# Kernel tuning notes

Hardware: AMD Instinct MI355X
Metric: run time of the kernel (lower is better)

## Reference

```python
import jax, jax.numpy as jnp
import numpy as np

B, S, E = 4, 2048, 1024
H = 16
DH = E // H  # per-head qk and v projection dim (64)


def setup_inputs() -> dict:
    key = jax.random.key(0)
    ks = jax.random.split(key, 12)
    sc = lambda fan_in: 1.0 / np.sqrt(fan_in)
    inp = {
        "query": jax.random.normal(ks[0], (B, S, E), jnp.float32),
        "key": jax.random.normal(ks[1], (B, S, E), jnp.float32),
        "value": jax.random.normal(ks[2], (B, S, E), jnp.float32),
        "attention_bias": jax.random.normal(ks[3], (S, S), jnp.float32),
        # stacked per-head Linear weights/biases (H independent heads in original)
        "Wq": jax.random.uniform(ks[4], (H, E, DH), jnp.float32, -sc(E), sc(E)),
        "bq": jax.random.uniform(ks[5], (H, DH), jnp.float32, -sc(E), sc(E)),
        "Wk": jax.random.uniform(ks[6], (H, E, DH), jnp.float32, -sc(E), sc(E)),
        "bk": jax.random.uniform(ks[7], (H, DH), jnp.float32, -sc(E), sc(E)),
        "Wv": jax.random.uniform(ks[8], (H, E, DH), jnp.float32, -sc(E), sc(E)),
        "bv": jax.random.uniform(ks[9], (H, DH), jnp.float32, -sc(E), sc(E)),
        "Wo": jax.random.uniform(ks[10], (H * DH, E), jnp.float32, -sc(H * DH), sc(H * DH)),
        "bo": jax.random.uniform(ks[11], (E,), jnp.float32, -sc(H * DH), sc(H * DH)),
    }
    return inp


def reference(query, key, value, attention_bias, Wq, bq, Wk, bk, Wv, bv, Wo, bo):
    # Batched equivalent of per-head Linear projections + per-head SDPA.
    q = jnp.einsum("bse,hed->bhsd", query, Wq) + bq[None, :, None, :]   # (B,H,S,DH)
    k = jnp.einsum("bte,hed->bhtd", key, Wk) + bk[None, :, None, :]     # (B,H,S,DH)
    v = jnp.einsum("bte,hed->bhtd", value, Wv) + bv[None, :, None, :]   # (B,H,S,DH)
    scale = 1.0 / jnp.sqrt(jnp.asarray(DH, q.dtype))
    scores = jnp.einsum("bhsd,bhtd->bhst", q, k) * scale                # (B,H,S,S)
    scores = scores + attention_bias[None, None, :, :]
    attn = jax.nn.softmax(scores, axis=-1)
    # dropout_p = 0.0 -> no dropout
    ctx = jnp.einsum("bhst,bhtd->bhsd", attn, v)                        # (B,H,S,DH)
    concat = ctx.transpose(0, 2, 1, 3).reshape(B, S, H * DH)            # (B,S,H*DH)
    return concat @ Wo + bo                                             # (B,S,E)
```

## Files before the change

### kernel.cpp

```cpp
#include <hip/hip_runtime.h>

#define S_LEN 2048
#define E_DIM 1024
#define H_NUM 16

typedef __attribute__((ext_vector_type(8))) short s16x8;
typedef __attribute__((ext_vector_type(4))) float f32x4;
typedef __attribute__((ext_vector_type(4))) _Float16 h16x4;
typedef __attribute__((ext_vector_type(8))) _Float16 h16x8;

#define GA(p) ((__attribute__((address_space(1))) void*)(p))
#define LA(p) ((__attribute__((address_space(3))) void*)(p))

#define LOG2E 1.4426950408889634f
#define SCALE_Q (0.125f * LOG2E)
#define SHIFT 12.0f

union cvt16 { int4 v; s16x8 s8; short e[8]; };

__device__ __forceinline__ short f2bf(float f) {
  union { float f; unsigned u; } v; v.f = f;
  unsigned r = v.u + 0x7FFFu + ((v.u >> 16) & 1u);
  return (short)(r >> 16);
}
__device__ __forceinline__ short f2bf_fast(float f) {
  union { float f; unsigned u; } v; v.f = f;
  return (short)((v.u + 0x8000u) >> 16);
}
__device__ __forceinline__ unsigned pk2(float lo, float hi) {
  return (unsigned)(unsigned short)f2bf_fast(lo) |
         ((unsigned)(unsigned short)f2bf_fast(hi) << 16);
}

__global__ void transpose_cast(const float* __restrict__ src, short* __restrict__ dst,
                               int R, int C, long sbs, long dbs, float scale) {
  __shared__ float tile[32][33];
  const float* s = src + (long)blockIdx.z * sbs;
  short* d = dst + (long)blockIdx.z * dbs;
  int c0 = blockIdx.x * 32, r0 = blockIdx.y * 32;
  #pragma unroll
  for (int i = threadIdx.y; i < 32; i += 8)
    tile[i][threadIdx.x] = s[(long)(r0 + i) * C + c0 + threadIdx.x];
  __syncthreads();
  #pragma unroll
  for (int i = threadIdx.y; i < 32; i += 8)
    d[(long)(c0 + i) * R + r0 + threadIdx.x] = f2bf(tile[threadIdx.x][i] * scale);
}

__global__ void bias_rearrange(const float* __restrict__ bias, _Float16* __restrict__ biasR) {
  long g = (long)blockIdx.x * 256 + threadIdx.x;
  int q    = (int)(g >> 8);
  int kv   = ((int)(g >> 3)) & 31;
  int quad = ((int)(g >> 1)) & 3;
  int c    = (int)g & 1;
  const float* src = bias + (long)q * 2048 + kv * 64 + c * 32 + quad * 4;
  f32x4 lo = *(const f32x4*)(src);
  f32x4 hi = *(const f32x4*)(src + 16);
  h16x8 hv;
  #pragma unroll
  for (int e = 0; e < 4; ++e) { hv[e] = (_Float16)lo[e]; hv[4 + e] = (_Float16)hi[e]; }
  *(h16x8*)(biasR + g * 8) = hv;
}

__global__ __launch_bounds__(256, 3) void proj_gemm(
    const float* __restrict__ Aq, const float* __restrict__ Ak, const float* __restrict__ Av,
    const short* __restrict__ Bt,
    const float* __restrict__ bq, const float* __restrict__ bk, const float* __restrict__ bv,
    short* __restrict__ qkOut, short* __restrict__ VT) {
  __shared__ float Asub[128 * 64];
  __shared__ short Bsub[128 * 64];
  const int tid = threadIdx.x;
  const int w = tid >> 6, lane = tid & 63, ln = lane & 15, quad = lane >> 4;
  const int row0 = blockIdx.x * 128, n0 = blockIdx.y * 128;
  const int seg = n0 >> 10;
  const float* A = (seg == 0) ? Aq : ((seg == 1) ? Ak : Av);
  const float* bptr = (seg == 0) ? bq : ((seg == 1) ? bk : bv);
  const float bscale = (seg == 0) ? SCALE_Q : 1.0f;
  const int nloc = n0 & 1023;
  const int wm = (w & 1) * 64, wn = (w >> 1) * 64;

  f32x4 acc[4][4];
  #pragma unroll
  for (int i = 0; i < 4; ++i)
    #pragma unroll
    for (int j = 0; j < 4; ++j) acc[i][j] = (f32x4){0.f, 0.f, 0.f, 0.f};

  for (int kt = 0; kt < 16; ++kt) {
    const int k0 = kt * 64;
    #pragma unroll
    for (int j = 0; j < 4; ++j) {
      int ci = (w * 4 + j) * 64 + lane;
      int r = ci >> 3, s = ci & 7, g = s ^ (r & 7);
      const short* gb = Bt + (long)(n0 + r) * 1024 + k0 + g * 8;
      __builtin_amdgcn_global_load_lds(GA(gb), LA(&Bsub[ci * 8]), 16, 0, 0);
    }
    #pragma unroll
    for (int it = 0; it < 8; ++it) {
      int ci = it * 256 + tid;
      int r = ci >> 4, s = ci & 15, g = (s & 8) | ((s & 7) ^ (r & 7));
      const float* ga = A + (long)(row0 + r) * 1024 + k0 + g * 4;
      __builtin_amdgcn_global_load_lds(GA(ga), LA(&Asub[ci * 4]), 16, 0, 0);
    }
    __syncthreads();
    #pragma unroll
    for (int kk = 0; kk < 2; ++kk) {
      s16x8 af[4], bfr[4];
      #pragma unroll
      for (int i = 0; i < 4; ++i) {
        int ra = wm + i * 16 + ln;
        int c0 = kk * 8 + quad * 2;
        int s0 = (c0 & 8) | ((c0 & 7) ^ (ra & 7));
        int c1 = c0 + 1;
        int s1 = (c1 & 8) | ((c1 & 7) ^ (ra & 7));
        f32x4 lo = *(const f32x4*)&Asub[ra * 64 + s0 * 4];
        f32x4 hi = *(const f32x4*)&Asub[ra * 64 + s1 * 4];
        s16x8 t;
        t[0] = f2bf(lo[0]); t[1] = f2bf(lo[1]); t[2] = f2bf(lo[2]); t[3] = f2bf(lo[3]);
        t[4] = f2bf(hi[0]); t[5] = f2bf(hi[1]); t[6] = f2bf(hi[2]); t[7] = f2bf(hi[3]);
        af[i] = t;
      }
      #pragma unroll
      for (int j = 0; j < 4; ++j) {
        int rb = wn + j * 16 + ln;
        int slot = (kk * 4 + quad) ^ (rb & 7);
        bfr[j] = *(const s16x8*)&Bsub[rb * 64 + slot * 8];
      }
      #pragma unroll
      for (int i = 0; i < 4; ++i)
        #pragma unroll
        for (int j = 0; j < 4; ++j)
          acc[i][j] = __builtin_amdgcn_mfma_f32_16x16x32_bf16(af[i], bfr[j], acc[i][j], 0, 0, 0);
    }
    __syncthreads();
  }
  if (seg < 2) {
    #pragma unroll
    for (int j = 0; j < 4; ++j) {
      float bvj = bptr[nloc + wn + j * 16 + ln] * bscale;
      int n = n0 + wn + j * 16 + ln;
      #pragma unroll
      for (int i = 0; i < 4; ++i)
        #pragma unroll
        for (int r = 0; r < 4; ++r) {
          int row = row0 + wm + i * 16 + quad * 4 + r;
          qkOut[(long)row * 2048 + n] = f2bf(acc[i][j][r] + bvj);
        }
    }
  } else {
    #pragma unroll
    for (int j = 0; j < 4; ++j) {
      int nl = nloc + wn + j * 16 + ln;
      int hh = nl >> 6, d = nl & 63;
      float bvj = bptr[nl];
      #pragma unroll
      for (int i = 0; i < 4; ++i) {
        int row = row0 + wm + i * 16 + quad * 4;
        int b = row >> 11, t = row & 2047;
        int u = t & 63;
        int pt = (t & ~63) | (u & 0x23) | ((u & 0x10) >> 2) | ((u & 0x0C) << 1);
        short4 sv;
        sv.x = f2bf(acc[i][j][0] + bvj);
        sv.y = f2bf(acc[i][j][1] + bvj);
        sv.z = f2bf(acc[i][j][2] + bvj);
        sv.w = f2bf(acc[i][j][3] + bvj);
        *(short4*)&VT[((long)(b * 16 + hh) * 64 + d) * 2048 + pt] = sv;
      }
    }
  }
}

__global__ __launch_bounds__(256, 3) void flash_attn(
    const short* __restrict__ qk, const short* __restrict__ VT,
    const _Float16* __restrict__ biasR, short* __restrict__ concat) {
  __shared__ short Ks[2][4096];
  __shared__ short Vs[2][4096];
  const int tid = threadIdx.x;
  const int w = tid >> 6, lane = tid & 63, ln = lane & 15, quad = lane >> 4;
  const int q0 = blockIdx.x * 128;
  const int h = blockIdx.y, bb = blockIdx.z;

  s16x8 ones;
  #pragma unroll
  for (int e = 0; e < 8; ++e) ones[e] = (short)0x3F80;

  s16x8 qf[2][2];
  const short* qbase = qk + (long)(bb * 2048 + q0 + w * 32) * 2048 + h * 64;
  #pragma unroll
  for (int i = 0; i < 2; ++i)
    #pragma unroll
    for (int kk = 0; kk < 2; ++kk) {
      cvt16 u; u.v = *(const int4*)(qbase + (long)(i * 16 + ln) * 2048 + kk * 32 + quad * 8);
      qf[i][kk] = u.s8;
    }

  f32x4 o[2][4], lacc[2];
  #pragma unroll
  for (int i = 0; i < 2; ++i) {
    #pragma unroll
    for (int nt = 0; nt < 4; ++nt) o[i][nt] = (f32x4){0.f, 0.f, 0.f, 0.f};
    lacc[i] = (f32x4){0.f, 0.f, 0.f, 0.f};
  }

  const short* kbase = qk + (long)bb * 2048 * 2048 + 1024 + h * 64;
  const short* vbase = VT + (long)(bb * 16 + h) * 64 * 2048;
  const _Float16* bbase = biasR + (long)(q0 + w * 32 + ln) * 2048 + quad * 16;

  #pragma unroll
  for (int j = 0; j < 2; ++j) {
    int ci = (w * 2 + j) * 64 + lane;
    int r = ci >> 3, cs = (ci & 7) ^ (r & 7);
    __builtin_amdgcn_global_load_lds(GA(kbase + (long)r * 2048 + cs * 8), LA(&Ks[0][(w * 2 + j) * 512]), 16, 0, 0);
    __builtin_amdgcn_global_load_lds(GA(vbase + (long)r * 2048 + cs * 8), LA(&Vs[0][(w * 2 + j) * 512]), 16, 0, 0);
  }

  for (int kv = 0; kv < 32; ++kv) {
    const int t0 = kv * 64, b = kv & 1;
    __syncthreads();

    h16x8 bld[2][2];
    #pragma unroll
    for (int i = 0; i < 2; ++i)
      #pragma unroll
      for (int c = 0; c < 2; ++c)
        bld[i][c] = *(const h16x8*)(bbase + (long)i * 16 * 2048 + kv * 64 + c * 8);
    __builtin_amdgcn_sched_barrier(0);

    if (kv < 31) {
      const short* kb = kbase + (long)(t0 + 64) * 2048;
      const short* vb = vbase + (t0 + 64);
      #pragma unroll
      for (int j = 0; j < 2; ++j) {
        int ci = (w * 2 + j) * 64 + lane;
        int r = ci >> 3, cs = (ci & 7) ^ (r & 7);
        __builtin_amdgcn_global_load_lds(GA(kb + (long)r * 2048 + cs * 8), LA(&Ks[b ^ 1][(w * 2 + j) * 512]), 16, 0, 0);
        __builtin_amdgcn_global_load_lds(GA(vb + (long)r * 2048 + cs * 8), LA(&Vs[b ^ 1][(w * 2 + j) * 512]), 16, 0, 0);
      }
    }

    f32x4 sa[2][4];
    #pragma unroll
    for (int i = 0; i < 2; ++i)
      #pragma unroll
      for (int nt = 0; nt < 4; ++nt) sa[i][nt] = (f32x4){-SHIFT, -SHIFT, -SHIFT, -SHIFT};
    #pragma unroll
    for (int kk = 0; kk < 2; ++kk) {
      s16x8 bfr[4];
      #pragma unroll
      for (int nt = 0; nt < 4; ++nt)
        bfr[nt] = *(const s16x8*)&Ks[b][((nt * 16 + ln) << 6) + (((kk * 4 + quad) ^ (ln & 7)) << 3)];
      __builtin_amdgcn_s_setprio(1);
      #pragma unroll
      for (int i = 0; i < 2; ++i)
        #pragma unroll
        for (int nt = 0; nt < 4; ++nt)
          sa[i][nt] = __builtin_amdgcn_mfma_f32_16x16x32_bf16(bfr[nt], qf[i][kk], sa[i][nt], 0, 0, 0);
      __builtin_amdgcn_s_setprio(0);
    }

    s16x8 pa[2][2];
    #pragma unroll
    for (int i = 0; i < 2; ++i) {
      #pragma unroll
      for (int nt = 0; nt < 4; ++nt) {
        #pragma unroll
        for (int r = 0; r < 4; ++r) {
          float bv = (float)bld[i][nt >> 1][(nt & 1) * 4 + r];
          sa[i][nt][r] = __builtin_amdgcn_exp2f(fmaf(bv, LOG2E, sa[i][nt][r]));
        }
      }
      #pragma unroll
      for (int kk = 0; kk < 2; ++kk) {
        union { unsigned u[4]; s16x8 v; } pw;
        pw.u[0] = pk2(sa[i][2 * kk][0], sa[i][2 * kk][1]);
        pw.u[1] = pk2(sa[i][2 * kk][2], sa[i][2 * kk][3]);
        pw.u[2] = pk2(sa[i][2 * kk + 1][0], sa[i][2 * kk + 1][1]);
        pw.u[3] = pk2(sa[i][2 * kk + 1][2], sa[i][2 * kk + 1][3]);
        pa[i][kk] = pw.v;
      }
    }

    #pragma unroll
    for (int kk = 0; kk < 2; ++kk) {
      s16x8 vbf[4];
      #pragma unroll
      for (int nt = 0; nt < 4; ++nt)
        vbf[nt] = *(const s16x8*)&Vs[b][((nt * 16 + ln) << 6) + (((kk * 4 + quad) ^ (ln & 7)) << 3)];
      __builtin_amdgcn_s_setprio(1);
      #pragma unroll
      for (int i = 0; i < 2; ++i) {
        #pragma unroll
        for (int nt = 0; nt < 4; ++nt)
          o[i][nt] = __builtin_amdgcn_mfma_f32_16x16x32_bf16(pa[i][kk], vbf[nt], o[i][nt], 0, 0, 0);
        lacc[i] = __builtin_amdgcn_mfma_f32_16x16x32_bf16(pa[i][kk], ones, lacc[i], 0, 0, 0);
      }
      __builtin_amdgcn_s_setprio(0);
    }
  }

  #pragma unroll
  for (int i = 0; i < 2; ++i) {
    float inv[4];
    #pragma unroll
    for (int r = 0; r < 4; ++r) inv[r] = __builtin_amdgcn_rcpf(lacc[i][r]);
    long rowb = (long)bb * 2048 + q0 + w * 32 + i * 16 + quad * 4;
    #pragma unroll
    for (int nt = 0; nt < 4; ++nt)
      #pragma unroll
      for (int r = 0; r < 4; ++r)
        concat[(rowb + r) * 1024 + h * 64 + nt * 16 + ln] = f2bf(o[i][nt][r] * inv[r]);
  }
}

__global__ __launch_bounds__(256, 3) void out_gemm(
    const short* __restrict__ A, const short* __restrict__ Bt,
    const float* __restrict__ bo, float* __restrict__ Cout) {
  __shared__ short Asub[128 * 64];
  __shared__ short Bsub[128 * 64];
  const int tid = threadIdx.x;
  const int w = tid >> 6, lane = tid & 63, ln = lane & 15, quad = lane >> 4;
  const int row0 = blockIdx.x * 128, n0 = blockIdx.y * 128;
  const int wm = (w & 1) * 64, wn = (w >> 1) * 64;

  f32x4 acc[4][4];
  #pragma unroll
  for (int i = 0; i < 4; ++i)
    #pragma unroll
    for (int j = 0; j < 4; ++j) acc[i][j] = (f32x4){0.f, 0.f, 0.f, 0.f};

  for (int kt = 0; kt < 16; ++kt) {
    const int k0 = kt * 64;
    #pragma unroll
    for (int j = 0; j < 4; ++j) {
      int ci = (w * 4 + j) * 64 + lane;
      int r = ci >> 3, s = ci & 7, g = s ^ (r & 7);
      const short* ga = A + (long)(row0 + r) * 1024 + k0 + g * 8;
      __builtin_amdgcn_global_load_lds(GA(ga), LA(&Asub[ci * 8]), 16, 0, 0);
      const short* gb = Bt + (long)(n0 + r) * 1024 + k0 + g * 8;
      __builtin_amdgcn_global_load_lds(GA(gb), LA(&Bsub[ci * 8]), 16, 0, 0);
    }
    __syncthreads();
    #pragma unroll
    for (int kk = 0; kk < 2; ++kk) {
      s16x8 af[4], bfr[4];
      #pragma unroll
      for (int i = 0; i < 4; ++i) {
        int ra = wm + i * 16 + ln;
        int slot = (kk * 4 + quad) ^ (ra & 7);
        af[i] = *(const s16x8*)&Asub[ra * 64 + slot * 8];
      }
      #pragma unroll
      for (int j = 0; j < 4; ++j) {
        int rb = wn + j * 16 + ln;
        int slot = (kk * 4 + quad) ^ (rb & 7);
        bfr[j] = *(const s16x8*)&Bsub[rb * 64 + slot * 8];
      }
      #pragma unroll
      for (int i = 0; i < 4; ++i)
        #pragma unroll
        for (int j = 0; j < 4; ++j)
          acc[i][j] = __builtin_amdgcn_mfma_f32_16x16x32_bf16(af[i], bfr[j], acc[i][j], 0, 0, 0);
    }
    __syncthreads();
  }
  #pragma unroll
  for (int j = 0; j < 4; ++j) {
    int n = n0 + wn + j * 16 + ln;
    float bvj = bo[n];
    #pragma unroll
    for (int i = 0; i < 4; ++i)
      #pragma unroll
      for (int r = 0; r < 4; ++r) {
        int row = row0 + wm + i * 16 + quad * 4 + r;
        Cout[(long)row * 1024 + n] = acc[i][j][r] + bvj;
      }
  }
}

extern "C" void kernel_launch(void* const* d_in, const int* in_sizes, int n_in,
                              void* d_out, int out_size, void* d_ws, size_t ws_size,
                              hipStream_t stream) {
  const float* query = (const float*)d_in[0];
  const float* key_  = (const float*)d_in[1];
  const float* value = (const float*)d_in[2];
  const float* abias = (const float*)d_in[3];
  const float* Wq = (const float*)d_in[4];
  const float* bq = (const float*)d_in[5];
  const float* Wk = (const float*)d_in[6];
  const float* bk = (const float*)d_in[7];
  const float* Wv = (const float*)d_in[8];
  const float* bv = (const float*)d_in[9];
  const float* Wo = (const float*)d_in[10];
  const float* bo = (const float*)d_in[11];
  float* out = (float*)d_out;

  char* ws = (char*)d_ws;
  short*    WqkvT  = (short*)(ws);
  _Float16* biasR  = (_Float16*)(ws);
  short*    qk     = (short*)(ws + 8388608);
  short*    VT     = (short*)(ws + 41943040);
  short*    WoT    = (short*)(ws + 41943040);
  short*    concat = (short*)(ws + 58720256);

  dim3 tb(32, 8);
  transpose_cast<<<dim3(2, 32, 16), tb, 0, stream>>>(Wq, WqkvT,           1024, 64, 65536L, 65536L, SCALE_Q);
  transpose_cast<<<dim3(2, 32, 16), tb, 0, stream>>>(Wk, WqkvT + 1048576, 1024, 64, 65536L, 65536L, 1.0f);
  transpose_cast<<<dim3(2, 32, 16), tb, 0, stream>>>(Wv, WqkvT + 2097152, 1024, 64, 65536L, 65536L, 1.0f);
  proj_gemm<<<dim3(64, 24), 256, 0, stream>>>(query, key_, value, WqkvT, bq, bk, bv, qk, VT);
  bias_rearrange<<<dim3(2048), 256, 0, stream>>>(abias, biasR);
  flash_attn<<<dim3(16, 16, 4), 256, 0, stream>>>(qk, VT, biasR, concat);
  transpose_cast<<<dim3(32, 32, 1), tb, 0, stream>>>(Wo, WoT, 1024, 1024, 0L, 0L, 1.0f);
  out_gemm<<<dim3(64, 8), 256, 0, stream>>>(concat, WoT, bo, out);
}
```

Baseline: 388.2 us.

## Replace ones-MFMA row sum with VALU sum, fold bias into accumulator init

Removes the extra MFMA per tile that multiplied P by a ones vector to get the softmax denominator. Each lane now adds up its fp32 exponentials, and the partial sums are combined through LDS once at the end. The attention bias is folded into the initial value of the score accumulator, and the manual bf16 rounding is replaced by the hardware v_cvt_pk_bf16_f32 packed convert. This cuts MFMA work per KV tile by one fifth in the PV stage, at the cost of extra VALU adds and an epilogue LDS reduction. The denominator now comes from unrounded fp32 values rather than the bf16-rounded P.

```diff
diff --git a/kernel.cpp b/kernel.cpp
--- a/kernel.cpp
+++ b/kernel.cpp
@@ -23,13 +23,10 @@
   unsigned r = v.u + 0x7FFFu + ((v.u >> 16) & 1u);
   return (short)(r >> 16);
 }
-__device__ __forceinline__ short f2bf_fast(float f) {
-  union { float f; unsigned u; } v; v.f = f;
-  return (short)((v.u + 0x8000u) >> 16);
-}
-__device__ __forceinline__ unsigned pk2(float lo, float hi) {
-  return (unsigned)(unsigned short)f2bf_fast(lo) |
-         ((unsigned)(unsigned short)f2bf_fast(hi) << 16);
+__device__ __forceinline__ unsigned pkc(float lo, float hi) {
+  unsigned r;
+  asm("v_cvt_pk_bf16_f32 %0, %1, %2" : "=v"(r) : "v"(lo), "v"(hi));
+  return r;
 }
 
 __global__ void transpose_cast(const float* __restrict__ src, short* __restrict__ dst,
@@ -179,10 +176,6 @@
   const int q0 = blockIdx.x * 128;
   const int h = blockIdx.y, bb = blockIdx.z;
 
-  s16x8 ones;
-  #pragma unroll
-  for (int e = 0; e < 8; ++e) ones[e] = (short)0x3F80;
-
   s16x8 qf[2][2];
   const short* qbase = qk + (long)(bb * 2048 + q0 + w * 32) * 2048 + h * 64;
   #pragma unroll
@@ -193,13 +186,12 @@
       qf[i][kk] = u.s8;
     }
 
-  f32x4 o[2][4], lacc[2];
-  #pragma unroll
-  for (int i = 0; i < 2; ++i) {
+  f32x4 o[2][4];
+  float lsum[2] = {0.f, 0.f};
+  #pragma unroll
+  for (int i = 0; i < 2; ++i)
     #pragma unroll
     for (int nt = 0; nt < 4; ++nt) o[i][nt] = (f32x4){0.f, 0.f, 0.f, 0.f};
-    lacc[i] = (f32x4){0.f, 0.f, 0.f, 0.f};
-  }
 
   const short* kbase = qk + (long)bb * 2048 * 2048 + 1024 + h * 64;
   const short* vbase = VT + (long)(bb * 16 + h) * 64 * 2048;
@@ -241,7 +233,11 @@
     #pragma unroll
     for (int i = 0; i < 2; ++i)
       #pragma unroll
-      for (int nt = 0; nt < 4; ++nt) sa[i][nt] = (f32x4){-SHIFT, -SHIFT, -SHIFT, -SHIFT};
+      for (int nt = 0; nt < 4; ++nt)
+        #pragma unroll
+        for (int r = 0; r < 4; ++r)
+          sa[i][nt][r] = fmaf((float)bld[i][nt >> 1][(nt & 1) * 4 + r], LOG2E, -SHIFT);
+
     #pragma unroll
     for (int kk = 0; kk < 2; ++kk) {
       s16x8 bfr[4];
@@ -261,20 +257,19 @@
     #pragma unroll
     for (int i = 0; i < 2; ++i) {
       #pragma unroll
-      for (int nt = 0; nt < 4; ++nt) {
-        #pragma unroll
-        for (int r = 0; r < 4; ++r) {
-          float bv = (float)bld[i][nt >> 1][(nt & 1) * 4 + r];
-          sa[i][nt][r] = __builtin_amdgcn_exp2f(fmaf(bv, LOG2E, sa[i][nt][r]));
-        }
-      }
+      for (int nt = 0; nt < 4; ++nt)
+        #pragma unroll
+        for (int r = 0; r < 4; ++r)
+          sa[i][nt][r] = __builtin_amdgcn_exp2f(sa[i][nt][r]);
+      f32x4 vs = (sa[i][0] + sa[i][1]) + (sa[i][2] + sa[i][3]);
+      lsum[i] += (vs[0] + vs[1]) + (vs[2] + vs[3]);
       #pragma unroll
       for (int kk = 0; kk < 2; ++kk) {
         union { unsigned u[4]; s16x8 v; } pw;
-        pw.u[0] = pk2(sa[i][2 * kk][0], sa[i][2 * kk][1]);
-        pw.u[1] = pk2(sa[i][2 * kk][2], sa[i][2 * kk][3]);
-        pw.u[2] = pk2(sa[i][2 * kk + 1][0], sa[i][2 * kk + 1][1]);
-        pw.u[3] = pk2(sa[i][2 * kk + 1][2], sa[i][2 * kk + 1][3]);
+        pw.u[0] = pkc(sa[i][2 * kk][0], sa[i][2 * kk][1]);
+        pw.u[1] = pkc(sa[i][2 * kk][2], sa[i][2 * kk][3]);
+        pw.u[2] = pkc(sa[i][2 * kk + 1][0], sa[i][2 * kk + 1][1]);
+        pw.u[3] = pkc(sa[i][2 * kk + 1][2], sa[i][2 * kk + 1][3]);
         pa[i][kk] = pw.v;
       }
     }
@@ -287,21 +282,28 @@
         vbf[nt] = *(const s16x8*)&Vs[b][((nt * 16 + ln) << 6) + (((kk * 4 + quad) ^ (ln & 7)) << 3)];
       __builtin_amdgcn_s_setprio(1);
       #pragma unroll
-      for (int i = 0; i < 2; ++i) {
+      for (int i = 0; i < 2; ++i)
         #pragma unroll
         for (int nt = 0; nt < 4; ++nt)
           o[i][nt] = __builtin_amdgcn_mfma_f32_16x16x32_bf16(pa[i][kk], vbf[nt], o[i][nt], 0, 0, 0);
-        lacc[i] = __builtin_amdgcn_mfma_f32_16x16x32_bf16(pa[i][kk], ones, lacc[i], 0, 0, 0);
-      }
       __builtin_amdgcn_s_setprio(0);
     }
   }
 
+  __syncthreads();
+  float* lred = (float*)&Ks[0][0];
+  #pragma unroll
+  for (int i = 0; i < 2; ++i)
+    lred[w * 128 + i * 64 + ln * 4 + quad] = lsum[i];
+  __syncthreads();
   #pragma unroll
   for (int i = 0; i < 2; ++i) {
     float inv[4];
     #pragma unroll
-    for (int r = 0; r < 4; ++r) inv[r] = __builtin_amdgcn_rcpf(lacc[i][r]);
+    for (int r = 0; r < 4; ++r) {
+      f32x4 lv = *(const f32x4*)&lred[w * 128 + i * 64 + (quad * 4 + r) * 4];
+      inv[r] = __builtin_amdgcn_rcpf((lv[0] + lv[1]) + (lv[2] + lv[3]));
+    }
     long rowb = (long)bb * 2048 + q0 + w * 32 + i * 16 + quad * 4;
     #pragma unroll
     for (int nt = 0; nt < 4; ++nt)
```

New measurement: 370.6 us. 4.5% less time.
